# Optimization experiments

Hardware: AMD Instinct MI355X
Metric: run time of the kernel (lower is better)

The kernel has to match this reference:

```python
import jax, jax.numpy as jnp
import numpy as np

B, N, OBS, ACT = 128, 32, 64, 16
D = OBS + ACT       # obs_z_input_dim = 80
H = 64              # hardcoded hidden width
WOUT = 64           # weight_output_dim (d_k_weight)
ZOUT = 64           # obs_z_output_dim (d_k_obsz)
FIN = OBS + ZOUT    # final_input_dim = 128
FOUT = 1            # final_output_dim


def _lin_params(key, fan_in, fan_out):
    k1, k2 = jax.random.split(key)
    w = jax.random.normal(k1, (fan_in, fan_out), jnp.float32) / np.sqrt(fan_in).astype(np.float32)
    b = jax.random.normal(k2, (fan_out,), jnp.float32) * 0.01
    return w, b


def setup_inputs() -> dict:
    key = jax.random.key(0)
    ks = jax.random.split(key, 16)
    inp = {
        "states": jax.random.normal(ks[0], (B, N, OBS), jnp.float32),
        "policies": jax.random.uniform(ks[1], (B, N, ACT), jnp.float32),
        "actions": jax.random.uniform(ks[2], (B, N, ACT), jnp.float32),
    }
    specs = [("kw", OBS, WOUT), ("qw", OBS, WOUT), ("ko", D, ZOUT),
             ("qo", D, ZOUT), ("av", D, ZOUT), ("fv", FIN, FOUT)]
    for idx, (nm, din, dout) in enumerate(specs):
        w1, b1 = _lin_params(ks[3 + 2 * idx], din, H)
        w2, b2 = _lin_params(ks[4 + 2 * idx], H, dout)
        inp[nm + "1_w"], inp[nm + "1_b"] = w1, b1
        inp[nm + "2_w"], inp[nm + "2_b"] = w2, b2
    return inp


def _mlp(x, w1, b1, w2, b2):
    return jax.nn.leaky_relu(x @ w1 + b1) @ w2 + b2


def reference(states, policies, actions,
              kw1_w, kw1_b, kw2_w, kw2_b,
              qw1_w, qw1_b, qw2_w, qw2_b,
              ko1_w, ko1_b, ko2_w, ko2_b,
              qo1_w, qo1_b, qo2_w, qo2_b,
              av1_w, av1_b, av2_w, av2_b,
              fv1_w, fv1_b, fv2_w, fv2_b):
    # --- mixing weight between taken actions and policies ---
    key_z = _mlp(states, kw1_w, kw1_b, kw2_w, kw2_b)    # [B,N,WOUT]
    query_z = _mlp(states, qw1_w, qw1_b, qw2_w, qw2_b)  # [B,N,WOUT]
    # torch: bmm(q, k^T).transpose(1,2) => weight_z[b,a,j] = sigmoid(q[b,j].k[b,a]/sqrt(dk))
    scores_z = jnp.einsum('bad,bjd->baj', key_z, query_z)
    weight_z = jax.nn.sigmoid(scores_z / np.float32(np.sqrt(WOUT)))[..., None]  # [B,N,N,1]

    # z[b,a,j] = w[b,a,j]*actions[b,j] + (1-w)*policies[b,j]
    z = weight_z * actions[:, None, :, :] + (1.0 - weight_z) * policies[:, None, :, :]  # [B,N,N,ACT]
    states_b = jnp.broadcast_to(states[:, None, :, :], (B, N, N, OBS))  # states_rep[b,a,j]=states[b,j]
    obs_z = jnp.concatenate([states_b, z], axis=-1)                     # [B,N,N,D]

    # source_obsz one-hot-diag trick selects obs_z[b,a,a] (broadcast over j)
    diag = jnp.arange(N)
    source = obs_z[:, diag, diag, :]                                    # [B,N,D]
    key_obsz = _mlp(source, ko1_w, ko1_b, ko2_w, ko2_b)                 # [B,N,ZOUT]
    query_obsz = _mlp(obs_z, qo1_w, qo1_b, qo2_w, qo2_b)                # [B,N,N,ZOUT]
    scores_obsz = jnp.sum(key_obsz[:, :, None, :] * query_obsz, axis=-1)  # [B,N,N]
    weight_obsz = jax.nn.softmax(scores_obsz / np.float32(np.sqrt(ZOUT)), axis=-1)
    ret_weight_obsz = weight_obsz[..., None]                            # [B,N,N,1]

    # obs_z_pi[b,a,k,j] = cat(states[b,j], policies[b,j]) if j==k else obs_z[b,a,j]
    # (place_zs / place_policies masking). The attention-value MLP is pointwise
    # over the last dim, so apply it to the two distinct branches and combine:
    vals = _mlp(obs_z, av1_w, av1_b, av2_w, av2_b)                      # [B,N,N,ZOUT]
    sp = jnp.concatenate([states, policies], axis=-1)                   # [B,N,D]
    vals_pi = _mlp(sp, av1_w, av1_b, av2_w, av2_b)                      # [B,N,ZOUT]

    w = weight_obsz  # broadcast weight w5[b,a,k,j] = w[b,a,j]
    sum_all = jnp.einsum('baj,bajd->bad', w, vals)                      # [B,N,ZOUT]
    node_features = (sum_all[:, :, None, :]
                     - w[..., None] * vals
                     + w[..., None] * vals_pi[:, None, :, :]) / N       # [B,N,N,ZOUT]

    node_in = jnp.concatenate([states_b, node_features], axis=-1)       # [B,N,N,FIN]
    value = _mlp(node_in, fv1_w, fv1_b, fv2_w, fv2_b)                   # [B,N,N,1]
    return value, weight_z, ret_weight_obsz
```

## Files before the change

kernel.cpp:

```cpp
#include <hip/hip_runtime.h>

#define NN   32
#define HID  64

typedef __attribute__((ext_vector_type(8))) short bf16x8;
typedef __attribute__((ext_vector_type(4))) float f32x4;
typedef unsigned short u16;
typedef unsigned int   u32;

__device__ __forceinline__ float leaky(float v) { return v >= 0.f ? v : 0.01f * v; }
__device__ __forceinline__ float wsum64(float p) {
#pragma unroll
    for (int o = 32; o; o >>= 1) p += __shfl_xor(p, o);
    return p;
}
__device__ __forceinline__ u16 f2bf(float f) {
    union { float f; u32 u; } v; v.f = f;
    return (u16)((v.u + 0x7FFFu + ((v.u >> 16) & 1)) >> 16);
}
__device__ __forceinline__ bf16x8 pack8(const float* v) {
    bf16x8 r;
#pragma unroll
    for (int e = 0; e < 8; ++e) r[e] = (short)f2bf(v[e]);
    return r;
}
__device__ __forceinline__ int swz(int row, int col)   { return row * 64 + ((((col >> 3) ^ (row & 7)) << 3) | (col & 7)); }
__device__ __forceinline__ int swz32(int row, int col) { return row * 32 + ((((col >> 3) ^ (row & 3)) << 3) | (col & 7)); }

__device__ __forceinline__ f32x4 gemm64(f32x4 C, const u16* A, const u16* W, int lm, int kb8, int bcol) {
#pragma unroll
    for (int k0 = 0; k0 < 64; k0 += 32) {
        const int g = (k0 >> 3) + kb8;
        const bf16x8 a = *(const bf16x8*)&A[lm * 64 + ((g ^ (lm & 7)) << 3)];
        const bf16x8 w = *(const bf16x8*)&W[bcol * 64 + ((g ^ (bcol & 7)) << 3)];
        C = __builtin_amdgcn_mfma_f32_16x16x32_bf16(a, w, C, 0, 0, 0);
    }
    return C;
}
__device__ __forceinline__ f32x4 gemm32(f32x4 C, const u16* A, const u16* W, int lm, int kb8, int bcol) {
    const bf16x8 a = *(const bf16x8*)&A[lm * 32 + ((kb8 ^ (lm & 3)) << 3)];
    const bf16x8 w = *(const bf16x8*)&W[bcol * 32 + ((kb8 ^ (bcol & 3)) << 3)];
    return __builtin_amdgcn_mfma_f32_16x16x32_bf16(a, w, C, 0, 0, 0);
}

#define W_KW1  0
#define W_KW2  4096
#define W_QW1  8192
#define W_QW2  12288
#define W_KO1A 16384
#define W_KO2  20480
#define W_QO2  24576
#define W_QO1A 28672
#define W_AV1A 32768
#define W_FV1A 36864
#define W_KO1B 40960
#define W_QO1B 43008
#define W_AV1B 45056

__global__ __launch_bounds__(256)
void prep_kernel(const float* __restrict__ av2_w, const float* __restrict__ av2_b,
                 const float* __restrict__ fv1_w,
                 const float* __restrict__ kw1_w, const float* __restrict__ kw2_w,
                 const float* __restrict__ qw1_w, const float* __restrict__ qw2_w,
                 const float* __restrict__ ko1_w, const float* __restrict__ ko2_w,
                 const float* __restrict__ qo2_w, const float* __restrict__ qo1_w,
                 const float* __restrict__ av1_w,
                 u16* __restrict__ MT, float* __restrict__ c, u16* __restrict__ wt)
{
    const int blk = blockIdx.x, t = threadIdx.x;
    if (blk == 0) {
        const int h = t & 63, jg = t >> 6;
        __shared__ float sA[4096];
        for (int i = t; i < 4096; i += 256) sA[i] = av2_w[i];
        __syncthreads();
        const float* W = fv1_w + 4096;
        float acc[16];
#pragma unroll
        for (int i = 0; i < 16; ++i) acc[i] = 0.f;
        for (int m = 0; m < 64; ++m) {
            const float w = W[m * 64 + h];
#pragma unroll
            for (int i = 0; i < 16; ++i)
                acc[i] = fmaf(sA[(jg + 4 * i) * 64 + m], w, acc[i]);
        }
#pragma unroll
        for (int i = 0; i < 16; ++i) { const int k = jg + 4 * i; MT[swz(h, k)] = f2bf(acc[i]); }
        if (t < 64) {
            float s = 0.f;
            for (int m = 0; m < 64; ++m) s = fmaf(av2_b[m], W[m * 64 + t], s);
            c[t] = s;
        }
    } else if (blk <= 9) {
        const float* srcs[9] = {kw1_w, kw2_w, qw1_w, qw2_w, ko1_w, ko2_w, qo1_w, av1_w, fv1_w};
        const int    offs[9] = {W_KW1, W_KW2, W_QW1, W_QW2, W_KO1A, W_KO2, W_QO1A, W_AV1A, W_FV1A};
        const float* W = srcs[blk - 1]; u16* dst = wt + offs[blk - 1];
        for (int i = t; i < 4096; i += 256) { const int k = i >> 6, h = i & 63; dst[swz(h, k)] = f2bf(W[i]); }
    } else if (blk == 10) {
        u16* dst = wt + W_QO2;
        for (int i = t; i < 4096; i += 256) { const int h = i >> 6, d = i & 63; dst[swz(h, d)] = f2bf(qo2_w[i]); }
    } else if (blk <= 13) {
        const float* srcs[3] = {ko1_w + 4096, qo1_w + 4096, av1_w + 4096};
        const int    offs[3] = {W_KO1B, W_QO1B, W_AV1B};
        const float* W = srcs[blk - 11]; u16* dst = wt + offs[blk - 11];
        for (int i = t; i < 1024; i += 256) {
            const int k = i >> 6, h = i & 63;
            dst[swz32(h, k)]      = f2bf(W[i]);
            dst[swz32(h, 16 + k)] = 0;
        }
    }
}

__global__ __launch_bounds__(256)
void setup_kernel(const float* __restrict__ states, const float* __restrict__ policies,
                  const float* __restrict__ actions,
                  const float* __restrict__ kw1_b, const float* __restrict__ kw2_b,
                  const float* __restrict__ qw1_b, const float* __restrict__ qw2_b,
                  const float* __restrict__ ko1_b, const float* __restrict__ ko2_b,
                  const float* __restrict__ qo1_b, const float* __restrict__ qo2_b,
                  const float* __restrict__ av1_b, const float* __restrict__ fv1_b,
                  const u16* __restrict__ wt, const u16* __restrict__ MT,
                  const float* __restrict__ c_,
                  u32* __restrict__ kzg, u32* __restrict__ qzg,
                  float* __restrict__ kq, float* __restrict__ kb,
                  float* __restrict__ baseq, float* __restrict__ deltaq,
                  float* __restrict__ basev, float* __restrict__ deltav,
                  float* __restrict__ pre, float* __restrict__ vpf)
{
    const int blk = blockIdx.x;
    const int row0 = blk * 16;
    const int t = threadIdx.x, lane = t & 63, jg = t >> 6;
    const int lm = lane & 15, kb8 = lane >> 4, cg = jg * 16 + lm;

    __shared__ __align__(16) u16 aST[1024], aH1[1024], aH2[1024], aKZ[1024], aQZ[1024];
    __shared__ __align__(16) u16 aP2[512], aDAP[512];
    __shared__ float fACT[256], fPOL[256];
    __shared__ float fKOBS[16 * 68];
    __shared__ float wzd[16];

    {
        const int i = t * 4, row = i >> 6, col = i & 63;
        const float4 s4 = *(const float4*)&states[row0 * 64 + i];
        const int base = swz(row, col);
        aST[base + 0] = f2bf(s4.x); aST[base + 1] = f2bf(s4.y);
        aST[base + 2] = f2bf(s4.z); aST[base + 3] = f2bf(s4.w);
        const float av = actions[row0 * 16 + t], pv = policies[row0 * 16 + t];
        fACT[t] = av; fPOL[t] = pv;
        const int r2 = t >> 4, cc = t & 15;
        aDAP[swz32(r2, cc)]      = f2bf(av - pv);
        aDAP[swz32(r2, 16 + cc)] = 0;
        aP2 [swz32(r2, 16 + cc)] = 0;
    }
    __syncthreads();

    {
        f32x4 C = {0.f,0.f,0.f,0.f};
        C = gemm64(C, aST, wt + W_KW1, lm, kb8, cg);
        const float bv = kw1_b[cg];
#pragma unroll
        for (int rr = 0; rr < 4; ++rr) aH1[swz(kb8 * 4 + rr, cg)] = f2bf(leaky(C[rr] + bv));
    }
    __syncthreads();

    {
        f32x4 C = {0.f,0.f,0.f,0.f};
        C = gemm64(C, aH1, wt + W_KW2, lm, kb8, cg);
        const float bv = kw2_b[cg];
#pragma unroll
        for (int rr = 0; rr < 4; ++rr) aKZ[swz(kb8 * 4 + rr, cg)] = f2bf(C[rr] + bv);
        f32x4 D = {0.f,0.f,0.f,0.f};
        D = gemm64(D, aST, wt + W_QW1, lm, kb8, cg);
        const float bq = qw1_b[cg];
#pragma unroll
        for (int rr = 0; rr < 4; ++rr) aH2[swz(kb8 * 4 + rr, cg)] = f2bf(leaky(D[rr] + bq));
    }
    __syncthreads();

    {
        f32x4 C = {0.f,0.f,0.f,0.f};
        C = gemm64(C, aH2, wt + W_QW2, lm, kb8, cg);
        const float bv = qw2_b[cg];
#pragma unroll
        for (int rr = 0; rr < 4; ++rr) aQZ[swz(kb8 * 4 + rr, cg)] = f2bf(C[rr] + bv);
    }
    __syncthreads();

    if (jg == 0) {
        f32x4 C = {0.f,0.f,0.f,0.f};
#pragma unroll
        for (int k0 = 0; k0 < 64; k0 += 32) {
            const int g = (k0 >> 3) + kb8;
            const bf16x8 a  = *(const bf16x8*)&aKZ[lm * 64 + ((g ^ (lm & 7)) << 3)];
            const bf16x8 qb = *(const bf16x8*)&aQZ[lm * 64 + ((g ^ (lm & 7)) << 3)];
            C = __builtin_amdgcn_mfma_f32_16x16x32_bf16(a, qb, C, 0, 0, 0);
        }
        if ((lm >> 2) == kb8) wzd[lm] = 1.f / (1.f + __expf(-C[lm & 3] * 0.125f));
    } else if (jg == 1) {
        const u32* s = (const u32*)aKZ;
        for (int i = lane; i < 512; i += 64) kzg[blk * 512 + i] = s[i];
    } else if (jg == 2) {
        const u32* s = (const u32*)aQZ;
        for (int i = lane; i < 512; i += 64) qzg[blk * 512 + i] = s[i];
    }
    __syncthreads();

    {
        const int r2 = t >> 4, cc = t & 15;
        const float w = wzd[r2];
        aP2[swz32(r2, cc)] = f2bf(w * fACT[t] + (1.f - w) * fPOL[t]);
    }
    __syncthreads();

    {
        f32x4 C = {0.f,0.f,0.f,0.f};
        C = gemm64(C, aST, wt + W_KO1A, lm, kb8, cg);
        C = gemm32(C, aP2, wt + W_KO1B, lm, kb8, cg);
        const float bv = ko1_b[cg];
#pragma unroll
        for (int rr = 0; rr < 4; ++rr) aH1[swz(kb8 * 4 + rr, cg)] = f2bf(leaky(C[rr] + bv));
    }
    __syncthreads();

    {
        f32x4 C = {0.f,0.f,0.f,0.f};
        C = gemm64(C, aH1, wt + W_KO2, lm, kb8, cg);
        const float bv = ko2_b[cg];
#pragma unroll
        for (int rr = 0; rr < 4; ++rr) {
            const float v = C[rr] + bv;
            aH2[swz(kb8 * 4 + rr, cg)] = f2bf(v);
            fKOBS[(kb8 * 4 + rr) * 68 + cg] = v;
        }
        const int r2 = t >> 4, cc = t & 15;
        aP2[swz32(r2, cc)] = f2bf(fPOL[t]);
    }
    __syncthreads();

    {
        f32x4 C = {0.f,0.f,0.f,0.f};
        C = gemm64(C, aH2, wt + W_QO2, lm, kb8, cg);
#pragma unroll
        for (int rr = 0; rr < 4; ++rr) kq[(row0 + kb8 * 4 + rr) * 64 + cg] = C[rr] * 0.125f;
    }
    {
        const float qb = qo2_b[lane];
#pragma unroll
        for (int q = 0; q < 4; ++q) {
            const int r = jg * 4 + q;
            const float s = wsum64(qb * fKOBS[r * 68 + lane]);
            if (lane == 0) kb[row0 + r] = s * 0.125f;
        }
    }
    {
        f32x4 C = {0.f,0.f,0.f,0.f};
        C = gemm64(C, aST, wt + W_QO1A, lm, kb8, cg);
        C = gemm32(C, aP2, wt + W_QO1B, lm, kb8, cg);
        const float bv = qo1_b[cg];
#pragma unroll
        for (int rr = 0; rr < 4; ++rr) baseq[(row0 + kb8 * 4 + rr) * 64 + cg] = C[rr] + bv;
    }
    {
        f32x4 C = {0.f,0.f,0.f,0.f};
        C = gemm32(C, aDAP, wt + W_QO1B, lm, kb8, cg);
#pragma unroll
        for (int rr = 0; rr < 4; ++rr) deltaq[(row0 + kb8 * 4 + rr) * 64 + cg] = C[rr];
    }
    {
        f32x4 C = {0.f,0.f,0.f,0.f};
        C = gemm64(C, aST, wt + W_AV1A, lm, kb8, cg);
        C = gemm32(C, aP2, wt + W_AV1B, lm, kb8, cg);
        const float bv = av1_b[cg];
#pragma unroll
        for (int rr = 0; rr < 4; ++rr) {
            const float v = C[rr] + bv;
            basev[(row0 + kb8 * 4 + rr) * 64 + cg] = v;
            aH1[swz(kb8 * 4 + rr, cg)] = f2bf(leaky(v));
        }
    }
    {
        f32x4 C = {0.f,0.f,0.f,0.f};
        C = gemm32(C, aDAP, wt + W_AV1B, lm, kb8, cg);
#pragma unroll
        for (int rr = 0; rr < 4; ++rr) deltav[(row0 + kb8 * 4 + rr) * 64 + cg] = C[rr];
    }
    {
        f32x4 C = {0.f,0.f,0.f,0.f};
        C = gemm64(C, aST, wt + W_FV1A, lm, kb8, cg);
        const float bv = fv1_b[cg];
#pragma unroll
        for (int rr = 0; rr < 4; ++rr) pre[(row0 + kb8 * 4 + rr) * 64 + cg] = C[rr] + bv;
    }
    __syncthreads();

    {
        f32x4 C = {0.f,0.f,0.f,0.f};
        C = gemm64(C, aH1, MT, lm, kb8, cg);
        const float bv = c_[cg];
#pragma unroll
        for (int rr = 0; rr < 4; ++rr) vpf[(row0 + kb8 * 4 + rr) * 64 + cg] = C[rr] + bv;
    }
}

__global__ __launch_bounds__(256)
void wz_kernel(const u32* __restrict__ kzg, const u32* __restrict__ qzg,
               float* __restrict__ out_wz)
{
    const int b = blockIdx.x, t = threadIdx.x, lane = t & 63, jg = t >> 6;
    __shared__ __align__(16) u16 sKZ[2048], sQZ[2048];
    u32* kzu = (u32*)sKZ; u32* qzu = (u32*)sQZ;
    for (int i = t; i < 1024; i += 256) { kzu[i] = kzg[b * 1024 + i]; qzu[i] = qzg[b * 1024 + i]; }
    __syncthreads();

    const int lm = lane & 15, kb8 = lane >> 4;
    const int rt = jg >> 1, ct = jg & 1;
    f32x4 acc = {0.f, 0.f, 0.f, 0.f};
#pragma unroll
    for (int k0 = 0; k0 < 64; k0 += 32) {
        const int g = (k0 >> 3) + kb8;
        const int ra = rt * 16 + lm, rb = ct * 16 + lm;
        const bf16x8 af = *(const bf16x8*)&sKZ[ra * 64 + ((g ^ (ra & 7)) << 3)];
        const bf16x8 bf = *(const bf16x8*)&sQZ[rb * 64 + ((g ^ (rb & 7)) << 3)];
        acc = __builtin_amdgcn_mfma_f32_16x16x32_bf16(af, bf, acc, 0, 0, 0);
    }
#pragma unroll
    for (int rr = 0; rr < 4; ++rr) {
        const int arow = rt * 16 + kb8 * 4 + rr;
        const int jcol = ct * 16 + lm;
        out_wz[b * 1024 + arow * 32 + jcol] = 1.f / (1.f + __expf(-acc[rr] * 0.125f));
    }
}

__global__ __launch_bounds__(256)
void main_kernel(const float* __restrict__ wz,
                 const float* __restrict__ kq,    const float* __restrict__ kb,
                 const float* __restrict__ baseq, const float* __restrict__ deltaq,
                 const float* __restrict__ basev, const float* __restrict__ deltav,
                 const float* __restrict__ pre,   const float* __restrict__ vpf,
                 const u16* __restrict__ MT,
                 const float* __restrict__ c,
                 const float* __restrict__ fv2_w, const float* __restrict__ fv2_b,
                 float* __restrict__ out_value,
                 float* __restrict__ out_wobs)
{
    const int bid0 = blockIdx.x;
    const int bid  = (bid0 & 7) * 512 + (bid0 >> 3);
    const int b = bid >> 5, a = bid & 31;
    const int t = threadIdx.x, lane = t & 63, jg = t >> 6;

    __shared__ __align__(16) short sHQ[2048];
    __shared__ __align__(16) short sHV[2048];
    __shared__ __align__(16) short sG[2048];
    __shared__ __align__(16) short sKQ16[64], sFV2[64];
    __shared__ float sC[32 * 65];
    __shared__ float sHBP[4 * 72];
    __shared__ float sHB[64], sCc[64];
    __shared__ float s_sc[NN], s_w[NN];

    if (t < 64) {
        sKQ16[t] = (short)f2bf(kq[(b * 32 + a) * 64 + t]);
        sFV2[t]  = (short)f2bf(fv2_w[t]);
        sCc[t]   = c[t];
    }
    const float kbv = kb[b * 32 + a];
    const int   row = t >> 3;
    const int   g2  = (t & 7) ^ (row & 7);
    const float wzv = wz[b * 1024 + a * 32 + row];
    {
        const int base = b * 2048 + t * 8;
        const float4 q0 = *(const float4*)&baseq[base],  q1 = *(const float4*)&baseq[base + 4];
        const float4 d0 = *(const float4*)&deltaq[base], d1 = *(const float4*)&deltaq[base + 4];
        const float4 v0 = *(const float4*)&basev[base],  v1 = *(const float4*)&basev[base + 4];
        const float4 e0 = *(const float4*)&deltav[base], e1 = *(const float4*)&deltav[base + 4];
        float hq[8], hv[8];
        hq[0]=leaky(q0.x+wzv*d0.x); hq[1]=leaky(q0.y+wzv*d0.y); hq[2]=leaky(q0.z+wzv*d0.z); hq[3]=leaky(q0.w+wzv*d0.w);
        hq[4]=leaky(q1.x+wzv*d1.x); hq[5]=leaky(q1.y+wzv*d1.y); hq[6]=leaky(q1.z+wzv*d1.z); hq[7]=leaky(q1.w+wzv*d1.w);
        hv[0]=leaky(v0.x+wzv*e0.x); hv[1]=leaky(v0.y+wzv*e0.y); hv[2]=leaky(v0.z+wzv*e0.z); hv[3]=leaky(v0.w+wzv*e0.w);
        hv[4]=leaky(v1.x+wzv*e1.x); hv[5]=leaky(v1.y+wzv*e1.y); hv[6]=leaky(v1.z+wzv*e1.z); hv[7]=leaky(v1.w+wzv*e1.w);
        *(bf16x8*)&sHQ[row * 64 + (g2 << 3)] = pack8(hq);
        *(bf16x8*)&sHV[row * 64 + (g2 << 3)] = pack8(hv);
    }
    __syncthreads();

    {
        const int lm = lane & 15, kb8 = lane >> 4;
        const int bcol = jg * 16 + lm;
        f32x4 acc0 = {0.f,0.f,0.f,0.f}, acc1 = {0.f,0.f,0.f,0.f}, accS = {0.f,0.f,0.f,0.f};
#pragma unroll
        for (int k0 = 0; k0 < 64; k0 += 32) {
            const int g = (k0 >> 3) + kb8;
            const bf16x8 bf = *(const bf16x8*)&MT[bcol * 64 + (((g ^ (bcol & 7)) << 3))];
            const int r0 = lm, r1 = 16 + lm;
            const bf16x8 a0 = *(const bf16x8*)&sHV[r0 * 64 + (((g ^ (r0 & 7)) << 3))];
            const bf16x8 a1 = *(const bf16x8*)&sHV[r1 * 64 + (((g ^ (r1 & 7)) << 3))];
            acc0 = __builtin_amdgcn_mfma_f32_16x16x32_bf16(a0, bf, acc0, 0, 0, 0);
            acc1 = __builtin_amdgcn_mfma_f32_16x16x32_bf16(a1, bf, acc1, 0, 0, 0);
            if (jg < 2) {
                const int rs = jg * 16 + lm;
                const bf16x8 aS = *(const bf16x8*)&sHQ[rs * 64 + (((g ^ (rs & 7)) << 3))];
                bf16x8 bS = {};
                if (lm == 0) bS = *(const bf16x8*)&sKQ16[k0 + kb8 * 8];
                accS = __builtin_amdgcn_mfma_f32_16x16x32_bf16(aS, bS, accS, 0, 0, 0);
            }
        }
#pragma unroll
        for (int rr = 0; rr < 4; ++rr) {
            sC[(kb8 * 4 + rr) * 65 + bcol]      = acc0[rr];
            sC[(16 + kb8 * 4 + rr) * 65 + bcol] = acc1[rr];
        }
        if (jg < 2 && lm == 0) {
#pragma unroll
            for (int rr = 0; rr < 4; ++rr)
                s_sc[jg * 16 + kb8 * 4 + rr] = accS[rr] + kbv;
        }
    }
    __syncthreads();

    float wreg;
    {
        const float sreg = s_sc[lane & 31];
        float m = sreg;
#pragma unroll
        for (int o = 1; o < 32; o <<= 1) m = fmaxf(m, __shfl_xor(m, o));
        const float e = __expf(sreg - m);
        float ssum = e;
#pragma unroll
        for (int o = 1; o < 32; o <<= 1) ssum += __shfl_xor(ssum, o);
        wreg = e / ssum;
        if (t < 32) { s_w[t] = wreg; out_wobs[b * 1024 + a * 32 + t] = wreg; }
        float p = 0.f;
#pragma unroll
        for (int jj = 0; jj < 8; ++jj) {
            const int j = jg * 8 + jj;
            p = fmaf(__shfl(wreg, j), sC[j * 65 + lane], p);
        }
        sHBP[jg * 72 + lane] = p;
    }
    __syncthreads();

    if (t < 64) sHB[t] = (sHBP[t] + sHBP[72 + t]) + (sHBP[144 + t] + sHBP[216 + t]);
    __syncthreads();

    {
        const int base = b * 2048 + t * 8;
        const float4 p0 = *(const float4*)&pre[base], p1 = *(const float4*)&pre[base + 4];
        const float4 f0 = *(const float4*)&vpf[base], f1 = *(const float4*)&vpf[base + 4];
        const float wrow = s_w[row];
        float preL[8] = {p0.x,p0.y,p0.z,p0.w,p1.x,p1.y,p1.z,p1.w};
        float vpfL[8] = {f0.x,f0.y,f0.z,f0.w,f1.x,f1.y,f1.z,f1.w};
        float gv[8];
#pragma unroll
        for (int e = 0; e < 8; ++e) {
            const int col = (t & 7) * 8 + e;
            const float g = preL[e] + (sHB[col] - wrow * sC[row * 65 + col]
                                       + (1.f - wrow) * sCc[col] + wrow * vpfL[e]) * (1.f / 32.f);
            gv[e] = leaky(g);
        }
        *(bf16x8*)&sG[row * 64 + (g2 << 3)] = pack8(gv);
    }
    __syncthreads();

    if (jg < 2) {
        const int lm = lane & 15, kb8 = lane >> 4;
        f32x4 accV = {0.f, 0.f, 0.f, 0.f};
#pragma unroll
        for (int k0 = 0; k0 < 64; k0 += 32) {
            const int g = (k0 >> 3) + kb8;
            const int rs = jg * 16 + lm;
            const bf16x8 aG = *(const bf16x8*)&sG[rs * 64 + (((g ^ (rs & 7)) << 3))];
            bf16x8 bF = {};
            if (lm == 0) bF = *(const bf16x8*)&sFV2[k0 + kb8 * 8];
            accV = __builtin_amdgcn_mfma_f32_16x16x32_bf16(aG, bF, accV, 0, 0, 0);
        }
        if (lm == 0) {
            const float fb2 = fv2_b[0];
#pragma unroll
            for (int rr = 0; rr < 4; ++rr)
                out_value[b * 1024 + a * 32 + jg * 16 + kb8 * 4 + rr] = accV[rr] + fb2;
        }
    }
}

extern "C" void kernel_launch(void* const* d_in, const int* in_sizes, int n_in,
                              void* d_out, int out_size, void* d_ws, size_t ws_size,
                              hipStream_t stream)
{
    const float* states   = (const float*)d_in[0];
    const float* policies = (const float*)d_in[1];
    const float* actions  = (const float*)d_in[2];
    const float* kw1_w = (const float*)d_in[3];  const float* kw1_b = (const float*)d_in[4];
    const float* kw2_w = (const float*)d_in[5];  const float* kw2_b = (const float*)d_in[6];
    const float* qw1_w = (const float*)d_in[7];  const float* qw1_b = (const float*)d_in[8];
    const float* qw2_w = (const float*)d_in[9];  const float* qw2_b = (const float*)d_in[10];
    const float* ko1_w = (const float*)d_in[11]; const float* ko1_b = (const float*)d_in[12];
    const float* ko2_w = (const float*)d_in[13]; const float* ko2_b = (const float*)d_in[14];
    const float* qo1_w = (const float*)d_in[15]; const float* qo1_b = (const float*)d_in[16];
    const float* qo2_w = (const float*)d_in[17]; const float* qo2_b = (const float*)d_in[18];
    const float* av1_w = (const float*)d_in[19]; const float* av1_b = (const float*)d_in[20];
    const float* av2_w = (const float*)d_in[21]; const float* av2_b = (const float*)d_in[22];
    const float* fv1_w = (const float*)d_in[23]; const float* fv1_b = (const float*)d_in[24];
    const float* fv2_w = (const float*)d_in[25]; const float* fv2_b = (const float*)d_in[26];

    float* out       = (float*)d_out;
    float* out_value = out;
    float* out_wz    = out + 131072;
    float* out_wobs  = out + 262144;

    const int SZ = 262144;
    float* ws   = (float*)d_ws;
    float* c_   = ws;
    float* kb_  = ws + 64;
    u16*   MT_  = (u16*)(ws + 4160);
    u32*   kzg  = (u32*)(ws + 6208);
    u32*   qzg  = (u32*)(ws + 137280);
    float* kq_   = ws + 268352;
    float* baseq = kq_   + SZ;
    float* dq_   = baseq + SZ;
    float* basev = dq_   + SZ;
    float* dv_   = basev + SZ;
    float* pre_  = dv_   + SZ;
    float* vpf_  = pre_  + SZ;
    u16*   wt_   = (u16*)(ws + 2103360);

    prep_kernel<<<14, 256, 0, stream>>>(
        av2_w, av2_b, fv1_w,
        kw1_w, kw2_w, qw1_w, qw2_w, ko1_w, ko2_w, qo2_w, qo1_w, av1_w,
        MT_, c_, wt_);

    setup_kernel<<<256, 256, 0, stream>>>(
        states, policies, actions,
        kw1_b, kw2_b, qw1_b, qw2_b, ko1_b, ko2_b, qo1_b, qo2_b, av1_b, fv1_b,
        wt_, MT_, c_,
        kzg, qzg, kq_, kb_, baseq, dq_, basev, dv_, pre_, vpf_);

    wz_kernel<<<128, 256, 0, stream>>>(kzg, qzg, out_wz);

    main_kernel<<<4096, 256, 0, stream>>>(
        out_wz, kq_, kb_, baseq, dq_, basev, dv_, pre_, vpf_,
        MT_, c_, fv2_w, fv2_b,
        out_value, out_wobs);
}
```

Baseline: 40.23 us.

## Replace degenerate MFMA dot-products with FP32 shuffle reductions and cut barriers in main kernel

After: 40.54 us. About the same (+0.8%).

```diff
diff --git a/kernel.cpp b/kernel.cpp
--- a/kernel.cpp
+++ b/kernel.cpp
@@ -345,45 +345,62 @@
     const int bid  = (bid0 & 7) * 512 + (bid0 >> 3);
     const int b = bid >> 5, a = bid & 31;
     const int t = threadIdx.x, lane = t & 63, jg = t >> 6;
-
-    __shared__ __align__(16) short sHQ[2048];
-    __shared__ __align__(16) short sHV[2048];
-    __shared__ __align__(16) short sG[2048];
-    __shared__ __align__(16) short sKQ16[64], sFV2[64];
+    const int row = t >> 3, s8 = t & 7, c0 = s8 * 8;
+
+    __shared__ __align__(16) u16 sHV[2048];
     __shared__ float sC[32 * 65];
-    __shared__ float sHBP[4 * 72];
-    __shared__ float sHB[64], sCc[64];
-    __shared__ float s_sc[NN], s_w[NN];
-
-    if (t < 64) {
-        sKQ16[t] = (short)f2bf(kq[(b * 32 + a) * 64 + t]);
-        sFV2[t]  = (short)f2bf(fv2_w[t]);
-        sCc[t]   = c[t];
-    }
+    __shared__ float sHB[64];
+    __shared__ float s_sc[NN];
+
+    const int base = b * 2048 + t * 8;
+    const float wzv = wz[b * 1024 + a * 32 + row];
     const float kbv = kb[b * 32 + a];
-    const int   row = t >> 3;
-    const int   g2  = (t & 7) ^ (row & 7);
-    const float wzv = wz[b * 1024 + a * 32 + row];
-    {
-        const int base = b * 2048 + t * 8;
+    const float4 p0 = *(const float4*)&pre[base], p1 = *(const float4*)&pre[base + 4];
+    const float4 f0 = *(const float4*)&vpf[base], f1 = *(const float4*)&vpf[base + 4];
+    {
         const float4 q0 = *(const float4*)&baseq[base],  q1 = *(const float4*)&baseq[base + 4];
         const float4 d0 = *(const float4*)&deltaq[base], d1 = *(const float4*)&deltaq[base + 4];
+        const float4 k0 = *(const float4*)&kq[(b * 32 + a) * 64 + c0];
+        const float4 k1 = *(const float4*)&kq[(b * 32 + a) * 64 + c0 + 4];
+        float p = leaky(q0.x + wzv * d0.x) * k0.x;
+        p = fmaf(leaky(q0.y + wzv * d0.y), k0.y, p);
+        p = fmaf(leaky(q0.z + wzv * d0.z), k0.z, p);
+        p = fmaf(leaky(q0.w + wzv * d0.w), k0.w, p);
+        p = fmaf(leaky(q1.x + wzv * d1.x), k1.x, p);
+        p = fmaf(leaky(q1.y + wzv * d1.y), k1.y, p);
+        p = fmaf(leaky(q1.z + wzv * d1.z), k1.z, p);
+        p = fmaf(leaky(q1.w + wzv * d1.w), k1.w, p);
+        p += __shfl_xor(p, 1); p += __shfl_xor(p, 2); p += __shfl_xor(p, 4);
+        if (s8 == 0) s_sc[row] = p + kbv;
+    }
+    {
         const float4 v0 = *(const float4*)&basev[base],  v1 = *(const float4*)&basev[base + 4];
         const float4 e0 = *(const float4*)&deltav[base], e1 = *(const float4*)&deltav[base + 4];
-        float hq[8], hv[8];
-        hq[0]=leaky(q0.x+wzv*d0.x); hq[1]=leaky(q0.y+wzv*d0.y); hq[2]=leaky(q0.z+wzv*d0.z); hq[3]=leaky(q0.w+wzv*d0.w);
-        hq[4]=leaky(q1.x+wzv*d1.x); hq[5]=leaky(q1.y+wzv*d1.y); hq[6]=leaky(q1.z+wzv*d1.z); hq[7]=leaky(q1.w+wzv*d1.w);
+        float hv[8];
         hv[0]=leaky(v0.x+wzv*e0.x); hv[1]=leaky(v0.y+wzv*e0.y); hv[2]=leaky(v0.z+wzv*e0.z); hv[3]=leaky(v0.w+wzv*e0.w);
         hv[4]=leaky(v1.x+wzv*e1.x); hv[5]=leaky(v1.y+wzv*e1.y); hv[6]=leaky(v1.z+wzv*e1.z); hv[7]=leaky(v1.w+wzv*e1.w);
-        *(bf16x8*)&sHQ[row * 64 + (g2 << 3)] = pack8(hq);
+        const int g2 = s8 ^ (row & 7);
         *(bf16x8*)&sHV[row * 64 + (g2 << 3)] = pack8(hv);
     }
     __syncthreads();
 
+    float wreg;
+    {
+        const float sreg = s_sc[lane & 31];
+        float m = sreg;
+#pragma unroll
+        for (int o = 1; o < 32; o <<= 1) m = fmaxf(m, __shfl_xor(m, o));
+        const float e = __expf(sreg - m);
+        float ssum = e;
+#pragma unroll
+        for (int o = 1; o < 32; o <<= 1) ssum += __shfl_xor(ssum, o);
+        wreg = e / ssum;
+        if (t < 32) out_wobs[b * 1024 + a * 32 + t] = wreg;
+    }
     {
         const int lm = lane & 15, kb8 = lane >> 4;
         const int bcol = jg * 16 + lm;
-        f32x4 acc0 = {0.f,0.f,0.f,0.f}, acc1 = {0.f,0.f,0.f,0.f}, accS = {0.f,0.f,0.f,0.f};
+        f32x4 acc0 = {0.f,0.f,0.f,0.f}, acc1 = {0.f,0.f,0.f,0.f};
 #pragma unroll
         for (int k0 = 0; k0 < 64; k0 += 32) {
             const int g = (k0 >> 3) + kb8;
@@ -393,89 +410,41 @@
             const bf16x8 a1 = *(const bf16x8*)&sHV[r1 * 64 + (((g ^ (r1 & 7)) << 3))];
             acc0 = __builtin_amdgcn_mfma_f32_16x16x32_bf16(a0, bf, acc0, 0, 0, 0);
             acc1 = __builtin_amdgcn_mfma_f32_16x16x32_bf16(a1, bf, acc1, 0, 0, 0);
-            if (jg < 2) {
-                const int rs = jg * 16 + lm;
-                const bf16x8 aS = *(const bf16x8*)&sHQ[rs * 64 + (((g ^ (rs & 7)) << 3))];
-                bf16x8 bS = {};
-                if (lm == 0) bS = *(const bf16x8*)&sKQ16[k0 + kb8 * 8];
-                accS = __builtin_amdgcn_mfma_f32_16x16x32_bf16(aS, bS, accS, 0, 0, 0);
-            }
-        }
+        }
+        float hb = 0.f;
 #pragma unroll
         for (int rr = 0; rr < 4; ++rr) {
-            sC[(kb8 * 4 + rr) * 65 + bcol]      = acc0[rr];
-            sC[(16 + kb8 * 4 + rr) * 65 + bcol] = acc1[rr];
-        }
-        if (jg < 2 && lm == 0) {
-#pragma unroll
-            for (int rr = 0; rr < 4; ++rr)
-                s_sc[jg * 16 + kb8 * 4 + rr] = accS[rr] + kbv;
-        }
-    }
-    __syncthreads();
-
-    float wreg;
-    {
-        const float sreg = s_sc[lane & 31];
-        float m = sreg;
-#pragma unroll
-        for (int o = 1; o < 32; o <<= 1) m = fmaxf(m, __shfl_xor(m, o));
-        const float e = __expf(sreg - m);
-        float ssum = e;
-#pragma unroll
-        for (int o = 1; o < 32; o <<= 1) ssum += __shfl_xor(ssum, o);
-        wreg = e / ssum;
-        if (t < 32) { s_w[t] = wreg; out_wobs[b * 1024 + a * 32 + t] = wreg; }
-        float p = 0.f;
-#pragma unroll
-        for (int jj = 0; jj < 8; ++jj) {
-            const int j = jg * 8 + jj;
-            p = fmaf(__shfl(wreg, j), sC[j * 65 + lane], p);
-        }
-        sHBP[jg * 72 + lane] = p;
-    }
-    __syncthreads();
-
-    if (t < 64) sHB[t] = (sHBP[t] + sHBP[72 + t]) + (sHBP[144 + t] + sHBP[216 + t]);
-    __syncthreads();
-
-    {
-        const int base = b * 2048 + t * 8;
-        const float4 p0 = *(const float4*)&pre[base], p1 = *(const float4*)&pre[base + 4];
-        const float4 f0 = *(const float4*)&vpf[base], f1 = *(const float4*)&vpf[base + 4];
-        const float wrow = s_w[row];
-        float preL[8] = {p0.x,p0.y,p0.z,p0.w,p1.x,p1.y,p1.z,p1.w};
-        float vpfL[8] = {f0.x,f0.y,f0.z,f0.w,f1.x,f1.y,f1.z,f1.w};
-        float gv[8];
+            const int r0 = kb8 * 4 + rr, r1 = 16 + kb8 * 4 + rr;
+            sC[r0 * 65 + bcol] = acc0[rr];
+            sC[r1 * 65 + bcol] = acc1[rr];
+            hb = fmaf(__shfl(wreg, r0), acc0[rr], hb);
+            hb = fmaf(__shfl(wreg, r1), acc1[rr], hb);
+        }
+        hb += __shfl_xor(hb, 16);
+        hb += __shfl_xor(hb, 32);
+        if (kb8 == 0 && jg == (bcol >> 4)) sHB[bcol] = hb;
+    }
+    __syncthreads();
+
+    {
+        const float wrow = __shfl(wreg, row);
+        const float4 cc0 = *(const float4*)&c[c0],     cc1 = *(const float4*)&c[c0 + 4];
+        const float4 fw0 = *(const float4*)&fv2_w[c0], fw1 = *(const float4*)&fv2_w[c0 + 4];
+        const float preL[8] = {p0.x,p0.y,p0.z,p0.w,p1.x,p1.y,p1.z,p1.w};
+        const float vpfL[8] = {f0.x,f0.y,f0.z,f0.w,f1.x,f1.y,f1.z,f1.w};
+        const float cL[8]   = {cc0.x,cc0.y,cc0.z,cc0.w,cc1.x,cc1.y,cc1.z,cc1.w};
+        const float fwL[8]  = {fw0.x,fw0.y,fw0.z,fw0.w,fw1.x,fw1.y,fw1.z,fw1.w};
+        float vpart = 0.f;
 #pragma unroll
         for (int e = 0; e < 8; ++e) {
-            const int col = (t & 7) * 8 + e;
-            const float g = preL[e] + (sHB[col] - wrow * sC[row * 65 + col]
-                                       + (1.f - wrow) * sCc[col] + wrow * vpfL[e]) * (1.f / 32.f);
-            gv[e] = leaky(g);
-        }
-        *(bf16x8*)&sG[row * 64 + (g2 << 3)] = pack8(gv);
-    }
-    __syncthreads();
-
-    if (jg < 2) {
-        const int lm = lane & 15, kb8 = lane >> 4;
-        f32x4 accV = {0.f, 0.f, 0.f, 0.f};
-#pragma unroll
-        for (int k0 = 0; k0 < 64; k0 += 32) {
-            const int g = (k0 >> 3) + kb8;
-            const int rs = jg * 16 + lm;
-            const bf16x8 aG = *(const bf16x8*)&sG[rs * 64 + (((g ^ (rs & 7)) << 3))];
-            bf16x8 bF = {};
-            if (lm == 0) bF = *(const bf16x8*)&sFV2[k0 + kb8 * 8];
-            accV = __builtin_amdgcn_mfma_f32_16x16x32_bf16(aG, bF, accV, 0, 0, 0);
-        }
-        if (lm == 0) {
-            const float fb2 = fv2_b[0];
-#pragma unroll
-            for (int rr = 0; rr < 4; ++rr)
-                out_value[b * 1024 + a * 32 + jg * 16 + kb8 * 4 + rr] = accV[rr] + fb2;
-        }
+            const int col = c0 + e;
+            float g = preL[e] + (sHB[col] - wrow * sC[row * 65 + col]
+                                 + (1.f - wrow) * cL[e] + wrow * vpfL[e]) * (1.f / 32.f);
+            g = leaky(g);
+            vpart = fmaf(g, fwL[e], vpart);
+        }
+        vpart += __shfl_xor(vpart, 1); vpart += __shfl_xor(vpart, 2); vpart += __shfl_xor(vpart, 4);
+        if (s8 == 0) out_value[b * 1024 + a * 32 + row] = vpart + fv2_b[0];
     }
 }
 
```
